# Optimization experiments

Hardware: AMD Instinct MI355X
Metric: run time of the kernel (lower is better)

## Reference

```python
import jax, jax.numpy as jnp
import numpy as np

N_NODES = 100000
N_EDGES = 1600000
NFEAT, NHID, NCLASS = 64, 128, 32


def _glorot(key, shape):
    fan_in, fan_out = shape[0], shape[1]
    lim = np.sqrt(6.0 / (fan_in + fan_out))
    return jax.random.uniform(key, shape, jnp.float32, -lim, lim)


def setup_inputs() -> dict:
    key = jax.random.key(0)
    ks = jax.random.split(key, 12)
    x = jax.random.normal(ks[0], (N_NODES, NFEAT), jnp.float32)
    edge_idx = jax.random.randint(ks[1], (2, N_EDGES), 0, N_NODES, jnp.int64)
    edge_weight = jax.random.uniform(ks[2], (N_EDGES,), jnp.float32)
    return {
        "x": x,
        "edge_idx": edge_idx,
        "edge_weight": edge_weight,
        # SAGEConv 1: out = mean_agg(x) @ Wl1 + b1 + x @ Wr1
        "Wl1": _glorot(ks[3], (NFEAT, NHID)),
        "Wr1": _glorot(ks[4], (NFEAT, NHID)),
        "b1": jnp.zeros((NHID,), jnp.float32),
        # SAGEConv 2
        "Wl2": _glorot(ks[5], (NHID, NHID)),
        "Wr2": _glorot(ks[6], (NHID, NHID)),
        "b2": jnp.zeros((NHID,), jnp.float32),
        # fc head: Linear(nhid, nclass) -> Linear(nclass, 1)
        "Wfc1": _glorot(ks[7], (NHID, NCLASS)),
        "bfc1": jnp.zeros((NCLASS,), jnp.float32),
        "Wfc2": _glorot(ks[8], (NCLASS, 1)),
        "bfc2": jnp.zeros((1,), jnp.float32),
    }


def _sage_conv(x, src, dst, Wl, Wr, b, n_nodes):
    # mean aggregation of source features at destination nodes
    msg_sum = jax.ops.segment_sum(x[src], dst, num_segments=n_nodes)  # [N, d]
    deg = jax.ops.segment_sum(jnp.ones((src.shape[0], 1), x.dtype), dst,
                              num_segments=n_nodes)                    # [N, 1]
    mean = msg_sum / jnp.maximum(deg, 1.0)
    return mean @ Wl + b + x @ Wr


def reference(x, edge_idx, edge_weight, Wl1, Wr1, b1, Wl2, Wr2, b2,
              Wfc1, bfc1, Wfc2, bfc2):
    n_nodes = x.shape[0]
    src, dst = edge_idx[0], edge_idx[1]
    # dropout is identity in eval mode (training=False)
    h = _sage_conv(x, src, dst, Wl1, Wr1, b1, n_nodes)   # [N, nhid]
    h = _sage_conv(h, src, dst, Wl2, Wr2, b2, n_nodes)   # [N, nhid]
    h = h @ Wfc1 + bfc1                                   # [N, nclass]
    out = h @ Wfc2 + bfc2                                 # [N, 1]
    return out
```

## Files before the change

### kernel.cpp

```cpp
#include <hip/hip_runtime.h>

#define S_SHIFT 7
#define S_NODES 128
#define NBKT    784
#define CAP     2560
#define CHUNK   8192
#define NREP    4
#define TPB     256
#define TOTAL_BLOCKS 1024

__global__ __launch_bounds__(TPB) void fused_kernel(
    const float* __restrict__ x,
    const int* __restrict__ src, const int* __restrict__ dst,
    int E, int N, int B, int nscat, int ndot,
    int* __restrict__ cursor, unsigned* __restrict__ bucket,
    const float* __restrict__ Wl1, const float* __restrict__ Wr1, const float* __restrict__ b1,
    const float* __restrict__ Wl2, const float* __restrict__ Wr2, const float* __restrict__ b2,
    const float* __restrict__ Wfc1, const float* __restrict__ bfc1,
    const float* __restrict__ Wfc2, const float* __restrict__ bfc2,
    float* __restrict__ ga, float2* __restrict__ gbc, float* __restrict__ c01)
{
    __shared__ int hist[NBKT], lbase[NBKT], lcur[NBKT];
    __shared__ __align__(16) float wv[192];
    __shared__ float uu[128], vl2[128], vr2[128], w2[32];
    int t = threadIdx.x;
    int l = t & 63;
    int w = t >> 6;
    int bid = blockIdx.x;

    if (bid < nscat) {
        int e0 = bid * CHUNK;
        int cnt = E - e0; if (cnt > CHUNK) cnt = CHUNK;
        for (int i = t; i < B; i += TPB) hist[i] = 0;
        __syncthreads();
        for (int i = t; i < cnt; i += TPB)
            atomicAdd(&hist[dst[e0 + i] >> S_SHIFT], 1);
        __syncthreads();
        for (int i = t; i < B; i += TPB) {
            lcur[i] = 0;
            if (hist[i] > 0) lbase[i] = atomicAdd(&cursor[i], hist[i]);
        }
        __syncthreads();
        for (int i = t; i < cnt; i += TPB) {
            int d = dst[e0 + i], s = src[e0 + i];
            int bb = d >> S_SHIFT;
            int off = atomicAdd(&lcur[bb], 1);
            bucket[(size_t)bb * CAP + (unsigned)(lbase[bb] + off)] =
                ((unsigned)s << S_SHIFT) | (unsigned)(d & (S_NODES - 1));
        }
    } else {
        if (t < 32) w2[t] = Wfc2[t];
        __syncthreads();
        for (int j = 0; j < 32; ++j) {
            int i = w + 4 * j;
            float p = (l < 32) ? Wfc1[i * 32 + l] * w2[l] : 0.f;
            for (int m = 16; m; m >>= 1) p += __shfl_xor(p, m);
            if (l == 0) uu[i] = p;
        }
        __syncthreads();
        for (int j = 0; j < 32; ++j) {
            int i = w + 4 * j;
            float ua = uu[l], ub = uu[64 + l];
            float pa = Wl2[i * 128 + l] * ua + Wl2[i * 128 + 64 + l] * ub;
            float pb = Wr2[i * 128 + l] * ua + Wr2[i * 128 + 64 + l] * ub;
            for (int m = 32; m; m >>= 1) { pa += __shfl_xor(pa, m); pb += __shfl_xor(pb, m); }
            if (l == 0) { vl2[i] = pa; vr2[i] = pb; }
        }
        __syncthreads();
        for (int j = 0; j < 16; ++j) {
            int i = w + 4 * j;
            float l1a = Wl1[i * 128 + l], l1b = Wl1[i * 128 + 64 + l];
            float r1a = Wr1[i * 128 + l], r1b = Wr1[i * 128 + 64 + l];
            float La = vl2[l], Lb = vl2[64 + l], Ra = vr2[l], Rb = vr2[64 + l];
            float pc = l1a * La + l1b * Lb;
            float pb = l1a * Ra + l1b * Rb + r1a * La + r1b * Lb;
            float pa = r1a * Ra + r1b * Rb;
            for (int m = 32; m; m >>= 1) {
                pa += __shfl_xor(pa, m); pb += __shfl_xor(pb, m); pc += __shfl_xor(pc, m);
            }
            if (l == 0) { wv[i] = pa; wv[64 + i] = pb; wv[128 + i] = pc; }
        }
        if (bid == nscat && w == 3) {
            float p0 = b1[l] * vr2[l] + b1[64 + l] * vr2[64 + l]
                     + b2[l] * uu[l] + b2[64 + l] * uu[64 + l];
            if (l < 32) p0 += bfc1[l] * w2[l];
            float p1 = b1[l] * vl2[l] + b1[64 + l] * vl2[64 + l];
            for (int m = 32; m; m >>= 1) { p0 += __shfl_xor(p0, m); p1 += __shfl_xor(p1, m); }
            if (l == 0) { c01[0] = p0 + bfc2[0]; c01[1] = p1; }
        }
        __syncthreads();

        int fp = l & 15, sub = l >> 4;
        float4 wa4 = ((const float4*)wv)[fp];
        float4 wb4 = ((const float4*)wv)[16 + fp];
        float4 wc4 = ((const float4*)wv)[32 + fp];
        const float4* x4 = (const float4*)x;
        int Q = (N + 3) >> 2;
        int wid = (bid - nscat) * (TPB / 64) + w;
        int stride = ndot * (TPB / 64);
        for (int qd = wid; qd < Q; qd += stride) {
            int node = qd * 4 + sub;
            float a = 0.f, b = 0.f, c = 0.f;
            if (node < N) {
                float4 v = x4[(size_t)node * 16 + fp];
                a = v.x * wa4.x + v.y * wa4.y + v.z * wa4.z + v.w * wa4.w;
                b = v.x * wb4.x + v.y * wb4.y + v.z * wb4.z + v.w * wb4.w;
                c = v.x * wc4.x + v.y * wc4.y + v.z * wc4.z + v.w * wc4.w;
            }
            for (int m = 8; m; m >>= 1) {
                a += __shfl_xor(a, m); b += __shfl_xor(b, m); c += __shfl_xor(c, m);
            }
            if (fp == 0 && node < N) { ga[node] = a; gbc[node] = make_float2(b, c); }
        }
    }
}

__global__ __launch_bounds__(TPB) void aggA_kernel(
    const unsigned* __restrict__ bucket, const int* __restrict__ cursor,
    const float2* __restrict__ gbc, const float* __restrict__ ga,
    const float* __restrict__ c01,
    float* __restrict__ q, float* __restrict__ t1, float* __restrict__ inv, int N)
{
    __shared__ float aB[NREP][S_NODES], aC[NREP][S_NODES];
    __shared__ int cnt[NREP][S_NODES];
    int t = threadIdx.x, b = blockIdx.x;
    int r = t >> 6;
    float* aBf = (float*)aB; float* aCf = (float*)aC; int* cnf = (int*)cnt;
    for (int i = t; i < NREP * S_NODES; i += TPB) { aBf[i] = 0.f; aCf[i] = 0.f; cnf[i] = 0; }
    __syncthreads();
    int n = cursor[b];
    const unsigned* bp = bucket + (size_t)b * CAP;
    int n4 = n & ~3;
    int i = 4 * t;
    bool have = i < n4;
    uint4 cur = make_uint4(0, 0, 0, 0);
    if (have) cur = *(const uint4*)(bp + i);
    while (have) {
        int in2 = i + 4 * TPB;
        bool hn = in2 < n4;
        uint4 nxt = cur;
        if (hn) nxt = *(const uint4*)(bp + in2);
        float2 g0 = gbc[cur.x >> S_SHIFT];
        float2 g1 = gbc[cur.y >> S_SHIFT];
        float2 g2 = gbc[cur.z >> S_SHIFT];
        float2 g3 = gbc[cur.w >> S_SHIFT];
        int d0 = cur.x & (S_NODES - 1), d1 = cur.y & (S_NODES - 1);
        int d2 = cur.z & (S_NODES - 1), d3 = cur.w & (S_NODES - 1);
        atomicAdd(&aB[r][d0], g0.x); atomicAdd(&aC[r][d0], g0.y); atomicAdd(&cnt[r][d0], 1);
        atomicAdd(&aB[r][d1], g1.x); atomicAdd(&aC[r][d1], g1.y); atomicAdd(&cnt[r][d1], 1);
        atomicAdd(&aB[r][d2], g2.x); atomicAdd(&aC[r][d2], g2.y); atomicAdd(&cnt[r][d2], 1);
        atomicAdd(&aB[r][d3], g3.x); atomicAdd(&aC[r][d3], g3.y); atomicAdd(&cnt[r][d3], 1);
        cur = nxt; i = in2; have = hn;
    }
    if (n4 + t < n) {
        unsigned uu = bp[n4 + t];
        float2 g = gbc[uu >> S_SHIFT];
        int dl = uu & (S_NODES - 1);
        atomicAdd(&aB[r][dl], g.x); atomicAdd(&aC[r][dl], g.y); atomicAdd(&cnt[r][dl], 1);
    }
    __syncthreads();
    if (t < S_NODES) {
        int node = (b << S_SHIFT) + t;
        if (node < N) {
            float sb = 0.f, sc = 0.f; int d = 0;
            #pragma unroll
            for (int k = 0; k < NREP; ++k) { sb += aB[k][t]; sc += aC[k][t]; d += cnt[k][t]; }
            float iv = 1.0f / ((d > 0) ? (float)d : 1.0f);
            inv[node] = iv;
            q[node]   = iv * sc;
            t1[node]  = ga[node] + iv * sb + c01[0] + (d > 0 ? c01[1] : 0.f);
        }
    }
}

__global__ __launch_bounds__(TPB) void aggB_kernel(
    const unsigned* __restrict__ bucket, const int* __restrict__ cursor,
    const float* __restrict__ q, const float* __restrict__ t1,
    const float* __restrict__ inv, float* __restrict__ out, int N)
{
    __shared__ float a2[NREP][S_NODES];
    int t = threadIdx.x, b = blockIdx.x;
    int r = t >> 6;
    float* a2f = (float*)a2;
    for (int i = t; i < NREP * S_NODES; i += TPB) a2f[i] = 0.f;
    __syncthreads();
    int n = cursor[b];
    const unsigned* bp = bucket + (size_t)b * CAP;
    int n4 = n & ~3;
    int i = 4 * t;
    bool have = i < n4;
    uint4 cur = make_uint4(0, 0, 0, 0);
    if (have) cur = *(const uint4*)(bp + i);
    while (have) {
        int in2 = i + 4 * TPB;
        bool hn = in2 < n4;
        uint4 nxt = cur;
        if (hn) nxt = *(const uint4*)(bp + in2);
        float q0 = q[cur.x >> S_SHIFT], q1 = q[cur.y >> S_SHIFT];
        float q2 = q[cur.z >> S_SHIFT], q3 = q[cur.w >> S_SHIFT];
        atomicAdd(&a2[r][cur.x & (S_NODES - 1)], q0);
        atomicAdd(&a2[r][cur.y & (S_NODES - 1)], q1);
        atomicAdd(&a2[r][cur.z & (S_NODES - 1)], q2);
        atomicAdd(&a2[r][cur.w & (S_NODES - 1)], q3);
        cur = nxt; i = in2; have = hn;
    }
    if (n4 + t < n) {
        unsigned uu = bp[n4 + t];
        atomicAdd(&a2[r][uu & (S_NODES - 1)], q[uu >> S_SHIFT]);
    }
    __syncthreads();
    if (t < S_NODES) {
        int node = (b << S_SHIFT) + t;
        if (node < N) {
            float s2 = 0.f;
            #pragma unroll
            for (int k = 0; k < NREP; ++k) s2 += a2[k][t];
            out[node] = t1[node] + inv[node] * s2;
        }
    }
}

extern "C" void kernel_launch(void* const* d_in, const int* in_sizes, int n_in,
                              void* d_out, int out_size, void* d_ws, size_t ws_size,
                              hipStream_t stream) {
    const float* x    = (const float*)d_in[0];
    const int*   eidx = (const int*)d_in[1];
    const float* Wl1  = (const float*)d_in[3];
    const float* Wr1  = (const float*)d_in[4];
    const float* b1   = (const float*)d_in[5];
    const float* Wl2  = (const float*)d_in[6];
    const float* Wr2  = (const float*)d_in[7];
    const float* b2   = (const float*)d_in[8];
    const float* Wfc1 = (const float*)d_in[9];
    const float* bfc1 = (const float*)d_in[10];
    const float* Wfc2 = (const float*)d_in[11];
    const float* bfc2 = (const float*)d_in[12];

    const int N = in_sizes[0] / 64;
    const int E = in_sizes[2];
    const int* src = eidx;
    const int* dst = eidx + E;
    const int B = (N + S_NODES - 1) >> S_SHIFT;
    const int nscat = (E + CHUNK - 1) / CHUNK;
    const int ndot = TOTAL_BLOCKS - nscat;

    char* ws = (char*)d_ws;
    int*      cursor = (int*)(ws);
    float*    c01    = (float*)(ws + 3200);
    float*    ga     = (float*)(ws + 4096);
    float*    q      = (float*)(ws + 4096 + (size_t)N * 4);
    float*    t1     = (float*)(ws + 4096 + (size_t)N * 8);
    float*    inv    = (float*)(ws + 4096 + (size_t)N * 12);
    float2*   gbc    = (float2*)(ws + 4096 + (size_t)N * 16);
    unsigned* bucket = (unsigned*)(ws + 4096 + (size_t)N * 24);

    hipMemsetAsync(cursor, 0, 3136, stream);

    fused_kernel<<<TOTAL_BLOCKS, TPB, 0, stream>>>(
        x, src, dst, E, N, B, nscat, ndot, cursor, bucket,
        Wl1, Wr1, b1, Wl2, Wr2, b2, Wfc1, bfc1, Wfc2, bfc2,
        ga, gbc, c01);

    aggA_kernel<<<B, TPB, 0, stream>>>(bucket, cursor, gbc, ga, c01, q, t1, inv, N);
    aggB_kernel<<<B, TPB, 0, stream>>>(bucket, cursor, q, t1, inv, (float*)d_out, N);
}
```

Baseline: 196.4 us.

## Compute degrees with global atomics in scatter phase, enlarge fused blocks

Per-node degree is now counted with global atomics on a zeroed deg array during the scatter histogram pass. This removes the per-edge shared-memory count atomics from aggA. The fused kernel moves to 512 threads per block with a fixed 160 dot-product blocks instead of filling up to 1024 blocks. The workspace is re-laid out with 128-byte alignment, and one memset clears both cursor and deg. The trade is 1.6M extra global atomics in the scatter phase and a larger memset, against lighter aggA inner loops.

Measured after the change: 227.3 us. 15.7% more time.

```diff
diff --git a/kernel.cpp b/kernel.cpp
--- a/kernel.cpp
+++ b/kernel.cpp
@@ -6,14 +6,15 @@
 #define CAP     2560
 #define CHUNK   8192
 #define NREP    4
-#define TPB     256
-#define TOTAL_BLOCKS 1024
-
-__global__ __launch_bounds__(TPB) void fused_kernel(
+#define FTH     512
+#define ATH     256
+#define NDOTS   160
+
+__global__ __launch_bounds__(FTH) void fused_kernel(
     const float* __restrict__ x,
     const int* __restrict__ src, const int* __restrict__ dst,
-    int E, int N, int B, int nscat, int ndot,
-    int* __restrict__ cursor, unsigned* __restrict__ bucket,
+    int E, int N, int B, int nscat,
+    int* __restrict__ cursor, int* __restrict__ deg, unsigned* __restrict__ bucket,
     const float* __restrict__ Wl1, const float* __restrict__ Wr1, const float* __restrict__ b1,
     const float* __restrict__ Wl2, const float* __restrict__ Wr2, const float* __restrict__ b2,
     const float* __restrict__ Wfc1, const float* __restrict__ bfc1,
@@ -31,17 +32,20 @@
     if (bid < nscat) {
         int e0 = bid * CHUNK;
         int cnt = E - e0; if (cnt > CHUNK) cnt = CHUNK;
-        for (int i = t; i < B; i += TPB) hist[i] = 0;
-        __syncthreads();
-        for (int i = t; i < cnt; i += TPB)
-            atomicAdd(&hist[dst[e0 + i] >> S_SHIFT], 1);
-        __syncthreads();
-        for (int i = t; i < B; i += TPB) {
+        for (int i = t; i < B; i += FTH) hist[i] = 0;
+        __syncthreads();
+        for (int i = t; i < cnt; i += FTH) {
+            int d = dst[e0 + i];
+            atomicAdd(&hist[d >> S_SHIFT], 1);
+            atomicAdd(&deg[d], 1);
+        }
+        __syncthreads();
+        for (int i = t; i < B; i += FTH) {
             lcur[i] = 0;
             if (hist[i] > 0) lbase[i] = atomicAdd(&cursor[i], hist[i]);
         }
         __syncthreads();
-        for (int i = t; i < cnt; i += TPB) {
+        for (int i = t; i < cnt; i += FTH) {
             int d = dst[e0 + i], s = src[e0 + i];
             int bb = d >> S_SHIFT;
             int off = atomicAdd(&lcur[bb], 1);
@@ -51,15 +55,15 @@
     } else {
         if (t < 32) w2[t] = Wfc2[t];
         __syncthreads();
-        for (int j = 0; j < 32; ++j) {
-            int i = w + 4 * j;
+        for (int j = 0; j < 16; ++j) {
+            int i = w + 8 * j;
             float p = (l < 32) ? Wfc1[i * 32 + l] * w2[l] : 0.f;
             for (int m = 16; m; m >>= 1) p += __shfl_xor(p, m);
             if (l == 0) uu[i] = p;
         }
         __syncthreads();
-        for (int j = 0; j < 32; ++j) {
-            int i = w + 4 * j;
+        for (int j = 0; j < 16; ++j) {
+            int i = w + 8 * j;
             float ua = uu[l], ub = uu[64 + l];
             float pa = Wl2[i * 128 + l] * ua + Wl2[i * 128 + 64 + l] * ub;
             float pb = Wr2[i * 128 + l] * ua + Wr2[i * 128 + 64 + l] * ub;
@@ -67,8 +71,8 @@
             if (l == 0) { vl2[i] = pa; vr2[i] = pb; }
         }
         __syncthreads();
-        for (int j = 0; j < 16; ++j) {
-            int i = w + 4 * j;
+        for (int j = 0; j < 8; ++j) {
+            int i = w + 8 * j;
             float l1a = Wl1[i * 128 + l], l1b = Wl1[i * 128 + 64 + l];
             float r1a = Wr1[i * 128 + l], r1b = Wr1[i * 128 + 64 + l];
             float La = vl2[l], Lb = vl2[64 + l], Ra = vr2[l], Rb = vr2[64 + l];
@@ -80,7 +84,7 @@
             }
             if (l == 0) { wv[i] = pa; wv[64 + i] = pb; wv[128 + i] = pc; }
         }
-        if (bid == nscat && w == 3) {
+        if (bid == nscat && w == 7) {
             float p0 = b1[l] * vr2[l] + b1[64 + l] * vr2[64 + l]
                      + b2[l] * uu[l] + b2[64 + l] * uu[64 + l];
             if (l < 32) p0 += bfc1[l] * w2[l];
@@ -96,9 +100,7 @@
         float4 wc4 = ((const float4*)wv)[32 + fp];
         const float4* x4 = (const float4*)x;
         int Q = (N + 3) >> 2;
-        int wid = (bid - nscat) * (TPB / 64) + w;
-        int stride = ndot * (TPB / 64);
-        for (int qd = wid; qd < Q; qd += stride) {
+        for (int qd = (bid - nscat) * 8 + w; qd < Q; qd += NDOTS * 8) {
             int node = qd * 4 + sub;
             float a = 0.f, b = 0.f, c = 0.f;
             if (node < N) {
@@ -115,18 +117,18 @@
     }
 }
 
-__global__ __launch_bounds__(TPB) void aggA_kernel(
+__global__ __launch_bounds__(ATH) void aggA_kernel(
     const unsigned* __restrict__ bucket, const int* __restrict__ cursor,
+    const int* __restrict__ deg,
     const float2* __restrict__ gbc, const float* __restrict__ ga,
     const float* __restrict__ c01,
     float* __restrict__ q, float* __restrict__ t1, float* __restrict__ inv, int N)
 {
     __shared__ float aB[NREP][S_NODES], aC[NREP][S_NODES];
-    __shared__ int cnt[NREP][S_NODES];
     int t = threadIdx.x, b = blockIdx.x;
     int r = t >> 6;
-    float* aBf = (float*)aB; float* aCf = (float*)aC; int* cnf = (int*)cnt;
-    for (int i = t; i < NREP * S_NODES; i += TPB) { aBf[i] = 0.f; aCf[i] = 0.f; cnf[i] = 0; }
+    float* aBf = (float*)aB; float* aCf = (float*)aC;
+    for (int i = t; i < NREP * S_NODES; i += ATH) { aBf[i] = 0.f; aCf[i] = 0.f; }
     __syncthreads();
     int n = cursor[b];
     const unsigned* bp = bucket + (size_t)b * CAP;
@@ -136,7 +138,7 @@
     uint4 cur = make_uint4(0, 0, 0, 0);
     if (have) cur = *(const uint4*)(bp + i);
     while (have) {
-        int in2 = i + 4 * TPB;
+        int in2 = i + 4 * ATH;
         bool hn = in2 < n4;
         uint4 nxt = cur;
         if (hn) nxt = *(const uint4*)(bp + in2);
@@ -146,25 +148,26 @@
         float2 g3 = gbc[cur.w >> S_SHIFT];
         int d0 = cur.x & (S_NODES - 1), d1 = cur.y & (S_NODES - 1);
         int d2 = cur.z & (S_NODES - 1), d3 = cur.w & (S_NODES - 1);
-        atomicAdd(&aB[r][d0], g0.x); atomicAdd(&aC[r][d0], g0.y); atomicAdd(&cnt[r][d0], 1);
-        atomicAdd(&aB[r][d1], g1.x); atomicAdd(&aC[r][d1], g1.y); atomicAdd(&cnt[r][d1], 1);
-        atomicAdd(&aB[r][d2], g2.x); atomicAdd(&aC[r][d2], g2.y); atomicAdd(&cnt[r][d2], 1);
-        atomicAdd(&aB[r][d3], g3.x); atomicAdd(&aC[r][d3], g3.y); atomicAdd(&cnt[r][d3], 1);
+        atomicAdd(&aB[r][d0], g0.x); atomicAdd(&aC[r][d0], g0.y);
+        atomicAdd(&aB[r][d1], g1.x); atomicAdd(&aC[r][d1], g1.y);
+        atomicAdd(&aB[r][d2], g2.x); atomicAdd(&aC[r][d2], g2.y);
+        atomicAdd(&aB[r][d3], g3.x); atomicAdd(&aC[r][d3], g3.y);
         cur = nxt; i = in2; have = hn;
     }
     if (n4 + t < n) {
         unsigned uu = bp[n4 + t];
         float2 g = gbc[uu >> S_SHIFT];
         int dl = uu & (S_NODES - 1);
-        atomicAdd(&aB[r][dl], g.x); atomicAdd(&aC[r][dl], g.y); atomicAdd(&cnt[r][dl], 1);
+        atomicAdd(&aB[r][dl], g.x); atomicAdd(&aC[r][dl], g.y);
     }
     __syncthreads();
     if (t < S_NODES) {
         int node = (b << S_SHIFT) + t;
         if (node < N) {
-            float sb = 0.f, sc = 0.f; int d = 0;
+            float sb = 0.f, sc = 0.f;
             #pragma unroll
-            for (int k = 0; k < NREP; ++k) { sb += aB[k][t]; sc += aC[k][t]; d += cnt[k][t]; }
+            for (int k = 0; k < NREP; ++k) { sb += aB[k][t]; sc += aC[k][t]; }
+            int d = deg[node];
             float iv = 1.0f / ((d > 0) ? (float)d : 1.0f);
             inv[node] = iv;
             q[node]   = iv * sc;
@@ -173,7 +176,7 @@
     }
 }
 
-__global__ __launch_bounds__(TPB) void aggB_kernel(
+__global__ __launch_bounds__(ATH) void aggB_kernel(
     const unsigned* __restrict__ bucket, const int* __restrict__ cursor,
     const float* __restrict__ q, const float* __restrict__ t1,
     const float* __restrict__ inv, float* __restrict__ out, int N)
@@ -182,7 +185,7 @@
     int t = threadIdx.x, b = blockIdx.x;
     int r = t >> 6;
     float* a2f = (float*)a2;
-    for (int i = t; i < NREP * S_NODES; i += TPB) a2f[i] = 0.f;
+    for (int i = t; i < NREP * S_NODES; i += ATH) a2f[i] = 0.f;
     __syncthreads();
     int n = cursor[b];
     const unsigned* bp = bucket + (size_t)b * CAP;
@@ -192,7 +195,7 @@
     uint4 cur = make_uint4(0, 0, 0, 0);
     if (have) cur = *(const uint4*)(bp + i);
     while (have) {
-        int in2 = i + 4 * TPB;
+        int in2 = i + 4 * ATH;
         bool hn = in2 < n4;
         uint4 nxt = cur;
         if (hn) nxt = *(const uint4*)(bp + in2);
@@ -242,25 +245,28 @@
     const int* dst = eidx + E;
     const int B = (N + S_NODES - 1) >> S_SHIFT;
     const int nscat = (E + CHUNK - 1) / CHUNK;
-    const int ndot = TOTAL_BLOCKS - nscat;
 
     char* ws = (char*)d_ws;
-    int*      cursor = (int*)(ws);
-    float*    c01    = (float*)(ws + 3200);
-    float*    ga     = (float*)(ws + 4096);
-    float*    q      = (float*)(ws + 4096 + (size_t)N * 4);
-    float*    t1     = (float*)(ws + 4096 + (size_t)N * 8);
-    float*    inv    = (float*)(ws + 4096 + (size_t)N * 12);
-    float2*   gbc    = (float2*)(ws + 4096 + (size_t)N * 16);
-    unsigned* bucket = (unsigned*)(ws + 4096 + (size_t)N * 24);
-
-    hipMemsetAsync(cursor, 0, 3136, stream);
-
-    fused_kernel<<<TOTAL_BLOCKS, TPB, 0, stream>>>(
-        x, src, dst, E, N, B, nscat, ndot, cursor, bucket,
+    size_t o = 0;
+    auto take = [&](size_t bytes) { char* p = ws + o; o += (bytes + 127) & ~(size_t)127; return p; };
+    int*      cursor = (int*)take(NBKT * 4);
+    int*      deg    = (int*)take((size_t)N * 4);
+    size_t zero_bytes = o;
+    float*    c01    = (float*)take(64);
+    float*    ga     = (float*)take((size_t)N * 4);
+    float*    q      = (float*)take((size_t)N * 4);
+    float*    t1     = (float*)take((size_t)N * 4);
+    float*    inv    = (float*)take((size_t)N * 4);
+    float2*   gbc    = (float2*)take((size_t)N * 8);
+    unsigned* bucket = (unsigned*)take((size_t)B * CAP * 4);
+
+    hipMemsetAsync(ws, 0, zero_bytes, stream);
+
+    fused_kernel<<<nscat + NDOTS, FTH, 0, stream>>>(
+        x, src, dst, E, N, B, nscat, cursor, deg, bucket,
         Wl1, Wr1, b1, Wl2, Wr2, b2, Wfc1, bfc1, Wfc2, bfc2,
         ga, gbc, c01);
 
-    aggA_kernel<<<B, TPB, 0, stream>>>(bucket, cursor, gbc, ga, c01, q, t1, inv, N);
-    aggB_kernel<<<B, TPB, 0, stream>>>(bucket, cursor, q, t1, inv, (float*)d_out, N);
-}
+    aggA_kernel<<<B, ATH, 0, stream>>>(bucket, cursor, deg, gbc, ga, c01, q, t1, inv, N);
+    aggB_kernel<<<B, ATH, 0, stream>>>(bucket, cursor, q, t1, inv, (float*)d_out, N);
+}
```
